# Kernel tuning notes

Hardware: AMD Instinct MI355X
Metric: run time of the kernel (lower is better)

Reference implementation:

```python
import jax, jax.numpy as jnp
import numpy as np

N_NODES = 100000
N_EDGES = 1600000
N_GRAPHS = 256
D_IN = 128
D_HID = 128
D_OUT = 10
N_GIN_LAYERS = 4  # num_layers - 1
BN_EPS = 1e-5


def setup_inputs() -> dict:
    key = jax.random.key(0)
    ks = jax.random.split(key, 16)
    x = jax.random.normal(ks[0], (N_NODES, D_IN), dtype=jnp.float32)
    edge_src = jax.random.randint(ks[1], (N_EDGES,), 0, N_NODES)
    edge_dst = jax.random.randint(ks[2], (N_EDGES,), 0, N_NODES)
    graph_ids = jnp.sort(jax.random.randint(ks[3], (N_NODES,), 0, N_GRAPHS))
    s = 1.0 / np.sqrt(D_HID)
    # stacked per-layer params (all layers 128->128 since input_dim == hidden_dim)
    W1 = jax.random.normal(ks[4], (N_GIN_LAYERS, D_HID, D_HID), dtype=jnp.float32) * s
    b1 = jnp.zeros((N_GIN_LAYERS, D_HID), dtype=jnp.float32)
    g1 = jnp.ones((N_GIN_LAYERS, D_HID), dtype=jnp.float32)
    bt1 = jnp.zeros((N_GIN_LAYERS, D_HID), dtype=jnp.float32)
    W2 = jax.random.normal(ks[5], (N_GIN_LAYERS, D_HID, D_HID), dtype=jnp.float32) * s
    b2 = jnp.zeros((N_GIN_LAYERS, D_HID), dtype=jnp.float32)
    g2 = jnp.ones((N_GIN_LAYERS, D_HID), dtype=jnp.float32)
    bt2 = jnp.zeros((N_GIN_LAYERS, D_HID), dtype=jnp.float32)
    eps = jnp.zeros((N_GIN_LAYERS,), dtype=jnp.float32)          # learn_eps params
    fusion_w = jnp.ones((N_GIN_LAYERS,), dtype=jnp.float32)      # self.weight
    Wp = jax.random.normal(ks[6], (D_HID, D_OUT), dtype=jnp.float32) * s
    bp = jnp.zeros((D_OUT,), dtype=jnp.float32)
    return {"x": x, "edge_src": edge_src, "edge_dst": edge_dst, "graph_ids": graph_ids,
            "eps": eps, "fusion_w": fusion_w, "W1": W1, "b1": b1, "g1": g1, "bt1": bt1,
            "W2": W2, "b2": b2, "g2": g2, "bt2": bt2, "Wp": Wp, "bp": bp}


def _batchnorm(h, gamma, beta):
    # training-mode BatchNorm1d over node axis
    m = jnp.mean(h, axis=0)
    v = jnp.var(h, axis=0)
    return (h - m) * jax.lax.rsqrt(v + BN_EPS) * gamma + beta


def reference(x, edge_src, edge_dst, graph_ids, eps, fusion_w,
              W1, b1, g1, bt1, W2, b2, g2, bt2, Wp, bp):
    h = x
    hiddens = []
    for l in range(N_GIN_LAYERS):
        # sum neighbor aggregation (spmm with learn_eps -> no self loops in Adj)
        pooled = jax.ops.segment_sum(h[edge_src], edge_dst, num_segments=N_NODES)
        pooled = pooled + (1.0 + eps[l]) * h
        # 2-layer MLP: Linear -> BN -> ReLU -> Linear
        t = jax.nn.relu(_batchnorm(pooled @ W1[l] + b1[l], g1[l], bt1[l]))
        t = t @ W2[l] + b2[l]
        # outer BatchNorm + ReLU
        h = jax.nn.relu(_batchnorm(t, g2[l], bt2[l]))
        hiddens.append(h)
    # attention_global, attention_type == 'weight': weighted sum of 4 hidden scales
    fused = (fusion_w[0] * hiddens[0] + fusion_w[1] * hiddens[1]
             + fusion_w[2] * hiddens[2] + fusion_w[3] * hiddens[3])
    # graph sum pooling (graph_pool spmm) then final linear (dropout = eval identity)
    pooled_g = jax.ops.segment_sum(fused, graph_ids, num_segments=N_GRAPHS)
    return pooled_g @ Wp + bp
```

## Files before the change

kernel.cpp:

```cpp
#include <hip/hip_runtime.h>

#define D 128
#define DOUT 10
#define CT_STRIDE 152
#define TSTR 136

typedef float f32x4 __attribute__((ext_vector_type(4)));
typedef __bf16 bf16x8 __attribute__((ext_vector_type(8)));
typedef unsigned short u16;

__device__ __forceinline__ float bf2f(u16 u) {
    return __uint_as_float(((unsigned int)u) << 16);
}
__device__ __forceinline__ u16 f2bf(float f) {
    unsigned int u = __float_as_uint(f);
    u += 0x7fffu + ((u >> 16) & 1u);
    return (u16)(u >> 16);
}

__global__ void k_zero(float4* __restrict__ p, int n4) {
    int i = blockIdx.x * 256 + threadIdx.x;
    if (i < n4) p[i] = make_float4(0.f, 0.f, 0.f, 0.f);
}

__global__ __launch_bounds__(256) void k_prepw(const float* __restrict__ W1,
                                               const float* __restrict__ W2,
                                               bf16x8* __restrict__ wswz, int L) {
    int b = blockIdx.x >> 3;
    const float* W = (b < L) ? (W1 + (size_t)b * D * D)
                             : (W2 + (size_t)(b - L) * D * D);
    bf16x8* o = wswz + (size_t)b * 2048;
    int idx = ((blockIdx.x & 7) << 8) + threadIdx.x;
    int lane_s = idx & 63;
    int f = idx >> 6;
    int n = ((f >> 2) << 4) | (lane_s & 15);
    int kb = ((f & 3) << 5) | ((lane_s >> 4) << 3);
    bf16x8 fr;
#pragma unroll
    for (int j = 0; j < 8; ++j) fr[j] = (__bf16)W[(kb + j) * D + n];
    o[idx] = fr;
}

__global__ __launch_bounds__(256) void k_hist(const int* __restrict__ dst,
                                              int* __restrict__ cnts, int E, int nb) {
    __shared__ int hist[1024];
    int tid = threadIdx.x;
    for (int i = tid; i < nb; i += 256) hist[i] = 0;
    __syncthreads();
    int e0 = blockIdx.x << 11;
    int e1 = e0 + 2048; if (e1 > E) e1 = E;
// ... 16 lines not shown
#pragma unroll
        for (int off = 1; off < 64; off <<= 1) {
            int v = __shfl_up(c, off);
            if (lane >= off) c += v;
        }
        if (idx < nbk) cnts[(idx << 10) + b] = carry + (c - orig);
        carry += __shfl(c, 63);
    }
    if (lane == 0) btot[b] = carry;
}

__global__ __launch_bounds__(256) void k_scat(const int* __restrict__ src,
                                              const int* __restrict__ dst,
                                              const int* __restrict__ cnts,
                                              int* __restrict__ pairs, int E, int nb) {
    __shared__ int lbase[1024];
    __shared__ int lcur[1024];
    int tid = threadIdx.x;
    for (int i = tid; i < nb; i += 256) {
        lbase[i] = cnts[(blockIdx.x << 10) + i];
        lcur[i] = 0;
    }
    __syncthreads();
    int e0 = blockIdx.x << 11;
    int e1 = e0 + 2048; if (e1 > E) e1 = E;
    for (int e = e0 + tid; e < e1; e += 256) {
        int d = dst[e];
        int b = d >> 7;
        int pos = lbase[b] + atomicAdd(&lcur[b], 1);
        if (pos < 4096) pairs[(b << 12) + pos] = (src[e] << 7) | (d & 127);
    }
}

__global__ void k_cvt(const float* __restrict__ x, u16* __restrict__ o,
                      int M, int Mpad) {
    long e = ((long)blockIdx.x * 256 + threadIdx.x) * 4;
    if (e >= (long)Mpad * D) return;
    ushort4 r;
    if (e < (long)M * D) {
        float4 v = *(const float4*)(x + e);
        r.x = f2bf(v.x); r.y = f2bf(v.y); r.z = f2bf(v.z); r.w = f2bf(v.w);
    } else {
        r = make_ushort4(0, 0, 0, 0);
    }
    *(ushort4*)(o + e) = r;
}

__global__ __launch_bounds__(512, 6) void k_aggemm(
        const u16* __restrict__ h, const int* __restrict__ pairs,
        const int* __restrict__ bcnt, const float* __restrict__ eps, int layer,
        const bf16x8* __restrict__ wz, const float* __restrict__ bias,
        u16* __restrict__ O, float* __restrict__ stats, int M, int b0) {
    __shared__ union UA {
        struct { int lcnt[128]; int loff[128]; int lcur[128]; int ledge[4096]; } csr;
        u16 tile[128 * TSTR];
    } shA;
    __shared__ float blds[D], psum[8 * D], psq[8 * D];
    int tid = threadIdx.x;

    if (tid < 128) shA.csr.lcnt[tid] = 0;
    if (tid >= 256 && tid < 256 + D) blds[tid - 256] = bias[tid - 256];
    __syncthreads();

    int b = b0 + blockIdx.x;
    int cnt = bcnt[b];
    if (cnt > 4096) cnt = 4096;
    const int* pb = pairs + ((size_t)b << 12);

    for (int e = tid; e < cnt; e += 512)
        atomicAdd(&shA.csr.lcnt[pb[e] & 127], 1);
    __syncthreads();
    if (tid < 128) shA.csr.loff[tid] = shA.csr.lcnt[tid];
    __syncthreads();
    for (int off = 1; off < 128; off <<= 1) {
        int v = 0;
        if (tid < 128 && tid >= off) v = shA.csr.loff[tid - off];
        __syncthreads();
        if (tid < 128) shA.csr.loff[tid] += v;
        __syncthreads();
    }
    if (tid < 128) shA.csr.lcur[tid] = shA.csr.loff[tid] - shA.csr.lcnt[tid];
    __syncthreads();
    for (int e = tid; e < cnt; e += 512) {
        int p = pb[e];
        int pos = atomicAdd(&shA.csr.lcur[p & 127], 1);
        shA.csr.ledge[pos] = p >> 7;
    }
    __syncthreads();

    float e1 = 1.0f + eps[layer];
    int grp = tid >> 5;
    int c = (tid & 31) << 2;
    float r0[8], r1[8], r2[8], r3[8];
    for (int pass = 0; pass < 8; ++pass) {
        int row = (pass << 4) + grp;
        int node = (b << 7) + row;
        float a0 = 0.f, a1 = 0.f, a2 = 0.f, a3 = 0.f;
        if (node < M) {
            ushort4 sv = *(const ushort4*)(h + ((size_t)node << 7) + c);
            a0 = e1 * bf2f(sv.x); a1 = e1 * bf2f(sv.y);
            a2 = e1 * bf2f(sv.z); a3 = e1 * bf2f(sv.w);
            int dd = shA.csr.lcnt[row];
            int s = shA.csr.loff[row] - dd;
            int i = 0;
            for (; i + 8 <= dd; i += 8) {
                int n0 = shA.csr.ledge[s + i],     n1 = shA.csr.ledge[s + i + 1];
                int n2 = shA.csr.ledge[s + i + 2], n3 = shA.csr.ledge[s + i + 3];
                int n4 = shA.csr.ledge[s + i + 4], n5 = shA.csr.ledge[s + i + 5];
                int n6 = shA.csr.ledge[s + i + 6], n7 = shA.csr.ledge[s + i + 7];
                ushort4 u0 = *(const ushort4*)(h + ((size_t)n0 << 7) + c);
                ushort4 u1 = *(const ushort4*)(h + ((size_t)n1 << 7) + c);
                ushort4 u2 = *(const ushort4*)(h + ((size_t)n2 << 7) + c);
                ushort4 u3 = *(const ushort4*)(h + ((size_t)n3 << 7) + c);
                ushort4 u4 = *(const ushort4*)(h + ((size_t)n4 << 7) + c);
                ushort4 u5 = *(const ushort4*)(h + ((size_t)n5 << 7) + c);
                ushort4 u6 = *(const ushort4*)(h + ((size_t)n6 << 7) + c);
                ushort4 u7 = *(const ushort4*)(h + ((size_t)n7 << 7) + c);
                a0 += bf2f(u0.x) + bf2f(u1.x) + bf2f(u2.x) + bf2f(u3.x)
                    + bf2f(u4.x) + bf2f(u5.x) + bf2f(u6.x) + bf2f(u7.x);
                a1 += bf2f(u0.y) + bf2f(u1.y) + bf2f(u2.y) + bf2f(u3.y)
                    + bf2f(u4.y) + bf2f(u5.y) + bf2f(u6.y) + bf2f(u7.y);
                a2 += bf2f(u0.z) + bf2f(u1.z) + bf2f(u2.z) + bf2f(u3.z)
                    + bf2f(u4.z) + bf2f(u5.z) + bf2f(u6.z) + bf2f(u7.z);
                a3 += bf2f(u0.w) + bf2f(u1.w) + bf2f(u2.w) + bf2f(u3.w)
                    + bf2f(u4.w) + bf2f(u5.w) + bf2f(u6.w) + bf2f(u7.w);
            }
            for (; i + 4 <= dd; i += 4) {
                int n0 = shA.csr.ledge[s + i],     n1 = shA.csr.ledge[s + i + 1];
                int n2 = shA.csr.ledge[s + i + 2], n3 = shA.csr.ledge[s + i + 3];
                ushort4 u0 = *(const ushort4*)(h + ((size_t)n0 << 7) + c);
                ushort4 u1 = *(const ushort4*)(h + ((size_t)n1 << 7) + c);
                ushort4 u2 = *(const ushort4*)(h + ((size_t)n2 << 7) + c);
                ushort4 u3 = *(const ushort4*)(h + ((size_t)n3 << 7) + c);
                a0 += bf2f(u0.x) + bf2f(u1.x) + bf2f(u2.x) + bf2f(u3.x);
                a1 += bf2f(u0.y) + bf2f(u1.y) + bf2f(u2.y) + bf2f(u3.y);
                a2 += bf2f(u0.z) + bf2f(u1.z) + bf2f(u2.z) + bf2f(u3.z);
                a3 += bf2f(u0.w) + bf2f(u1.w) + bf2f(u2.w) + bf2f(u3.w);
            }
            for (; i < dd; ++i) {
                int n0 = shA.csr.ledge[s + i];
                ushort4 u0 = *(const ushort4*)(h + ((size_t)n0 << 7) + c);
                a0 += bf2f(u0.x); a1 += bf2f(u0.y); a2 += bf2f(u0.z); a3 += bf2f(u0.w);
            }
        }
        r0[pass] = a0; r1[pass] = a1; r2[pass] = a2; r3[pass] = a3;
    }
    __syncthreads();

#pragma unroll
    for (int pass = 0; pass < 8; ++pass) {
        int row = (pass << 4) + grp;
        ushort4 v;
        v.x = f2bf(r0[pass]); v.y = f2bf(r1[pass]);
        v.z = f2bf(r2[pass]); v.w = f2bf(r3[pass]);
        *(ushort4*)&shA.tile[row * TSTR + c] = v;
    }
    __syncthreads();

    int wave = tid >> 6, lane = tid & 63;
    int m = lane & 15, quad = lane >> 4;
    f32x4 z = {0.f, 0.f, 0.f, 0.f};
    f32x4 acc[8];
#pragma unroll
    for (int t = 0; t < 8; ++t) acc[t] = z;
    const bf16x8* wl = wz + lane;
#pragma unroll
    for (int kc = 0; kc < 4; ++kc) {
        bf16x8 af = *(const bf16x8*)&shA.tile[(wave * 16 + m) * TSTR + (kc << 5) + (quad << 3)];
        bf16x8 w0 = wl[(0  | kc) << 6];
        bf16x8 w1 = wl[(4  | kc) << 6];
        bf16x8 w2 = wl[(8  | kc) << 6];
        bf16x8 w3 = wl[(12 | kc) << 6];
        acc[0] = __builtin_amdgcn_mfma_f32_16x16x32_bf16(af, w0, acc[0], 0, 0, 0);
        acc[1] = __builtin_amdgcn_mfma_f32_16x16x32_bf16(af, w1, acc[1], 0, 0, 0);
        acc[2] = __builtin_amdgcn_mfma_f32_16x16x32_bf16(af, w2, acc[2], 0, 0, 0);
        acc[3] = __builtin_amdgcn_mfma_f32_16x16x32_bf16(af, w3, acc[3], 0, 0, 0);
        w0 = wl[(16 | kc) << 6];
        w1 = wl[(20 | kc) << 6];
        w2 = wl[(24 | kc) << 6];
        w3 = wl[(28 | kc) << 6];
        acc[4] = __builtin_amdgcn_mfma_f32_16x16x32_bf16(af, w0, acc[4], 0, 0, 0);
        acc[5] = __builtin_amdgcn_mfma_f32_16x16x32_bf16(af, w1, acc[5], 0, 0, 0);
        acc[6] = __builtin_amdgcn_mfma_f32_16x16x32_bf16(af, w2, acc[6], 0, 0, 0);
        acc[7] = __builtin_amdgcn_mfma_f32_16x16x32_bf16(af, w3, acc[7], 0, 0, 0);
    }
    __syncthreads();

    int lr0 = wave * 16 + (quad << 2);
    int gr0 = (b << 7) + lr0;
#pragma unroll
    for (int t = 0; t < 8; ++t) {
        int cch = (t << 4) | m;
        float bc = blds[cch];
        float s = 0.f, q = 0.f;
#pragma unroll
        for (int r = 0; r < 4; ++r) {
            float v = acc[t][r] + bc;
            shA.tile[(lr0 + r) * TSTR + cch] = f2bf(v);
            if (gr0 + r < M) { s += v; q += v * v; }
        }
        s += __shfl_xor(s, 16); s += __shfl_xor(s, 32);
        q += __shfl_xor(q, 16); q += __shfl_xor(q, 32);
        if (quad == 0) { psum[wave * D + cch] = s; psq[wave * D + cch] = q; }
    }
    __syncthreads();

    int mrow = M - (b << 7);
#pragma unroll
    for (int i = 0; i < 4; ++i) {
        int idx = (i << 9) + tid;
        int row = idx >> 4, ch8 = (idx & 15) << 3;
        if (row < mrow) {
            float4 v = *(const float4*)&shA.tile[row * TSTR + ch8];
            *(float4*)(O + (((size_t)(b << 7) + row) << 7) + ch8) = v;
        }
    }
    if (tid < D) {
        float s = 0.f, q = 0.f;
#pragma unroll
        for (int w = 0; w < 8; ++w) { s += psum[w * D + tid]; q += psq[w * D + tid]; }
        float* st = stats + ((b & 7) << 8);
        atomicAdd(&st[tid], s);
        atomicAdd(&st[D + tid], q);
    }
}

__global__ __launch_bounds__(256, 4) void k_gemm_bn(
        u16* __restrict__ A, const bf16x8* __restrict__ wz,
        const float* __restrict__ bias, const float* __restrict__ stats_in,
        const float* __restrict__ gamma, const float* __restrict__ beta,
        float* __restrict__ stats_out, float invM, int M) {
    __shared__ union { bf16x8 w[2048]; u16 c[64 * CT_STRIDE]; } sh;
    __shared__ float blds[D], s_sc[D], s_sh[D], psum[4 * D], psq[4 * D];
    int tid = threadIdx.x;
    int wave = tid >> 6, lane = tid & 63;
    int m = lane & 15, quad = lane >> 4;
    int row0 = blockIdx.x * 64 + wave * 16;

    const u16* ap = A + (size_t)(row0 + m) * D + (quad << 3);
    ushort4 p[4][2];
#pragma unroll
    for (int kc = 0; kc < 4; ++kc) {
        p[kc][0] = *(const ushort4*)(ap + (kc << 5));
        p[kc][1] = *(const ushort4*)(ap + (kc << 5) + 4);
    }

    for (int i = tid; i < 2048; i += 256) sh.w[i] = wz[i];
    if (tid < D) {
        float s = 0.f, q = 0.f;
#pragma unroll
        for (int r = 0; r < 8; ++r) {
            s += stats_in[(r << 8) + tid];
            q += stats_in[(r << 8) + D + tid];
        }
        float mean = s * invM;
        float var = q * invM - mean * mean;
        float sc = rsqrtf(var + 1e-5f) * gamma[tid];
        s_sc[tid] = sc;
        s_sh[tid] = beta[tid] - mean * sc;
        blds[tid] = bias[tid];
    }
    __syncthreads();

    f32x4 z = {0.f, 0.f, 0.f, 0.f};
    f32x4 acc[8];
#pragma unroll
    for (int t = 0; t < 8; ++t) acc[t] = z;

#pragma unroll
    for (int kc = 0; kc < 4; ++kc) {
        int kb = (kc << 5) | (quad << 3);
        float4 c0 = *(const float4*)&s_sc[kb];
// ... 13 lines not shown
#pragma unroll
        for (int t = 0; t < 8; ++t)
            acc[t] = __builtin_amdgcn_mfma_f32_16x16x32_bf16(
                af, sh.w[(((t << 2) | kc) << 6) | lane], acc[t], 0, 0, 0);
    }
    __syncthreads();

    int lr0 = wave * 16 + (quad << 2);
    int gr0 = blockIdx.x * 64 + lr0;
#pragma unroll
    for (int t = 0; t < 8; ++t) {
        int cch = (t << 4) | m;
        float bc = blds[cch];
        float s = 0.f, q = 0.f;
#pragma unroll
        for (int r = 0; r < 4; ++r) {
            float v = acc[t][r] + bc;
            sh.c[(lr0 + r) * CT_STRIDE + cch] = f2bf(v);
            if (gr0 + r < M) { s += v; q += v * v; }
        }
        s += __shfl_xor(s, 16); s += __shfl_xor(s, 32);
        q += __shfl_xor(q, 16); q += __shfl_xor(q, 32);
        if (quad == 0) { psum[wave * D + cch] = s; psq[wave * D + cch] = q; }
    }
    __syncthreads();

    int mrow = M - blockIdx.x * 64;
#pragma unroll
    for (int i = 0; i < 4; ++i) {
        int idx = (i << 8) + tid;
        int row = idx >> 4, ch8 = (idx & 15) << 3;
        if (row < mrow) {
            float4 v = *(const float4*)&sh.c[row * CT_STRIDE + ch8];
            *(float4*)(A + ((size_t)(blockIdx.x * 64 + row) << 7) + ch8) = v;
        }
    }
    if (tid < D) {
        float s = psum[tid] + psum[D + tid] + psum[2 * D + tid] + psum[3 * D + tid];
        float q = psq[tid] + psq[D + tid] + psq[2 * D + tid] + psq[3 * D + tid];
        float* st = stats_out + ((blockIdx.x & 7) << 8);
        atomicAdd(&st[tid], s);
        atomicAdd(&st[D + tid], q);
    }
}

__global__ __launch_bounds__(256) void k_bn2pool(
        const u16* __restrict__ y, const float* __restrict__ stats,
        const float* __restrict__ gamma, const float* __restrict__ beta,
        const int* __restrict__ gids, const float* __restrict__ fw,
        int layer, u16* __restrict__ hout, float* __restrict__ gacc,
        float invM, int M) {
    __shared__ float s_sc[D], s_sh[D];
    int t = threadIdx.x;
    if (t < D) {
        float s = 0.f, q = 0.f;
#pragma unroll
        for (int r = 0; r < 8; ++r) {
            s += stats[(r << 8) + t];
            q += stats[(r << 8) + D + t];
        }
        float mean = s * invM;
        float sv = rsqrtf(q * invM - mean * mean + 1e-5f) * gamma[t];
        s_sc[t] = sv;
        s_sh[t] = beta[t] - mean * sv;
    }
    __syncthreads();

    int c = (t & 31) << 2;
    int strip = t >> 5;
    long base = (long)blockIdx.x * 64 + (long)strip * 8;
    if (base >= M) return;
    float4 sc4 = *(const float4*)&s_sc[c];
    float4 sh4 = *(const float4*)&s_sh[c];

    ushort4 v[8];
#pragma unroll
    for (int r = 0; r < 8; ++r)
        v[r] = *(const ushort4*)(y + ((base + r) << 7) + c);
    long gmax = (long)M - 1;
    int g[8];
#pragma unroll
    for (int r = 0; r < 8; ++r) {
        long idx = base + r;
        g[r] = gids[idx > gmax ? gmax : idx];
    }

    float h0[8], h1[8], h2[8], h3[8];
#pragma unroll
    for (int r = 0; r < 8; ++r) {
        h0[r] = fmaxf(0.f, fmaf(bf2f(v[r].x), sc4.x, sh4.x));
        h1[r] = fmaxf(0.f, fmaf(bf2f(v[r].y), sc4.y, sh4.y));
        h2[r] = fmaxf(0.f, fmaf(bf2f(v[r].z), sc4.z, sh4.z));
        h3[r] = fmaxf(0.f, fmaf(bf2f(v[r].w), sc4.w, sh4.w));
    }
#pragma unroll
    for (int r = 0; r < 8; ++r) {
        if (base + r < M) {
            ushort4 o;
            o.x = f2bf(h0[r]); o.y = f2bf(h1[r]);
            o.z = f2bf(h2[r]); o.w = f2bf(h3[r]);
            *(ushort4*)(hout + ((base + r) << 7) + c) = o;
        }
    }

    float wl = fw[layer];
    int cur = -1;
    float a0 = 0.f, a1 = 0.f, a2 = 0.f, a3 = 0.f;
#pragma unroll
    for (int r = 0; r < 8; ++r) {
        if (base + r < M) {
            if (g[r] != cur) {
                if (cur >= 0) {
                    float* gp = gacc + ((size_t)cur << 7) + c;
                    atomicAdd(gp, wl * a0); atomicAdd(gp + 1, wl * a1);
                    atomicAdd(gp + 2, wl * a2); atomicAdd(gp + 3, wl * a3);
                }
                cur = g[r];
                a0 = a1 = a2 = a3 = 0.f;
            }
            a0 += h0[r]; a1 += h1[r]; a2 += h2[r]; a3 += h3[r];
        }
    }
    if (cur >= 0) {
        float* gp = gacc + ((size_t)cur << 7) + c;
        atomicAdd(gp, wl * a0); atomicAdd(gp + 1, wl * a1);
        atomicAdd(gp + 2, wl * a2); atomicAdd(gp + 3, wl * a3);
    }
}

__global__ void k_final(const float* __restrict__ gacc, const float* __restrict__ Wp,
                        const float* __restrict__ bp, float* __restrict__ out) {
    __shared__ float w[D * DOUT];
    __shared__ float bb[DOUT];
    int t = threadIdx.x;
    for (int i = t; i < D * DOUT; i += blockDim.x) w[i] = Wp[i];
    if (t < DOUT) bb[t] = bp[t];
    __syncthreads();
    float acc[DOUT];
#pragma unroll
    for (int o = 0; o < DOUT; ++o) acc[o] = bb[o];
    for (int k = 0; k < D; ++k) {
        float a = gacc[(size_t)t * D + k];
#pragma unroll
        for (int o = 0; o < DOUT; ++o) acc[o] += a * w[k * DOUT + o];
    }
#pragma unroll
    for (int o = 0; o < DOUT; ++o) out[(size_t)t * DOUT + o] = acc[o];
}

extern "C" void kernel_launch(void* const* d_in, const int* in_sizes, int n_in,
                              void* d_out, int out_size, void* d_ws, size_t ws_size,
                              hipStream_t stream) {
    const float* x    = (const float*)d_in[0];
    const int* esrc   = (const int*)d_in[1];
    const int* edst   = (const int*)d_in[2];
    const int* gids   = (const int*)d_in[3];
    const float* eps  = (const float*)d_in[4];
    const float* fw   = (const float*)d_in[5];
    const float* W1   = (const float*)d_in[6];
    const float* b1   = (const float*)d_in[7];
    const float* g1   = (const float*)d_in[8];
    const float* bt1  = (const float*)d_in[9];
    const float* W2   = (const float*)d_in[10];
    const float* b2   = (const float*)d_in[11];
    const float* g2   = (const float*)d_in[12];
    const float* bt2  = (const float*)d_in[13];
    const float* Wp   = (const float*)d_in[14];
    const float* bp   = (const float*)d_in[15];
    float* out        = (float*)d_out;

    const int M = in_sizes[3];
    const int E = in_sizes[1];
    const int L = in_sizes[4];
    const int G = out_size / DOUT;
    const int nb  = (M + 127) >> 7;
    const int Mpad = nb << 7;
    const int nbk = (E + 2047) >> 11;
    const float invM = 1.0f / (float)M;

    char* ws = (char*)d_ws;
    u16* bufT  = (u16*)ws;  ws += (size_t)Mpad * D * 2;
    u16* bufH  = (u16*)ws;  ws += (size_t)Mpad * D * 2;
    int* pairs = (int*)ws;  ws += (size_t)nb * 4096 * 4;
    int* cnts  = (int*)ws;  ws += (size_t)nbk * 1024 * 4;
    int* btot  = (int*)ws;  ws += 1024 * 4;
    bf16x8* wswz = (bf16x8*)ws; ws += (size_t)2 * L * 2048 * 16;
    float* stats = (float*)ws; ws += (size_t)L * 4096 * 4;
    float* gacc  = (float*)ws; ws += (size_t)G * D * 4;

    int zbytes = L * 4096 * 4 + G * D * 4;
    int n4 = zbytes / 16;
    k_zero<<<(n4 + 255) / 256, 256, 0, stream>>>((float4*)stats, n4);

    k_prepw<<<2 * L * 8, 256, 0, stream>>>(W1, W2, wswz, L);
    k_hist<<<nbk, 256, 0, stream>>>(edst, cnts, E, nb);
    k_off<<<(nb + 3) / 4, 256, 0, stream>>>(cnts, btot, nbk, nb);
    k_scat<<<nbk, 256, 0, stream>>>(esrc, edst, cnts, pairs, E, nb);
    k_cvt<<<(Mpad * (D / 4) + 255) / 256, 256, 0, stream>>>(x, bufH, M, Mpad);

    int pool_grid = (M + 63) / 64;
    for (int l = 0; l < L; ++l) {
        float* st1 = stats + (size_t)l * 4096;
        float* st2 = st1 + 2048;
        k_aggemm<<<nb, 512, 0, stream>>>(bufH, pairs, btot, eps, l,
                                         wswz + (size_t)l * 2048, b1 + (size_t)l * D,
                                         bufT, st1, M, 0);
        k_gemm_bn<<<Mpad / 64, 256, 0, stream>>>(bufT, wswz + (size_t)(L + l) * 2048,
                                                 b2 + (size_t)l * D, st1,
                                                 g1 + (size_t)l * D, bt1 + (size_t)l * D,
                                                 st2, invM, M);
        k_bn2pool<<<pool_grid, 256, 0, stream>>>(bufT, st2, g2 + (size_t)l * D,
                                                 bt2 + (size_t)l * D, gids, fw, l,
                                                 bufH, gacc, invM, M);
    }
    k_final<<<1, G, 0, stream>>>(gacc, Wp, bp, out);
}
```

Measured before the change: 758.0 us.

## Fuse outer BatchNorm+ReLU and graph pooling into next layer's aggregation kernel

The separate BN2+ReLU+pool kernel is removed for all but the last layer. Its work moves into the next layer's aggregation gather, which now applies the previous layer's scale/shift and ReLU to each gathered neighbor row on the fly and accumulates graph pooling from self rows. k_gemm_bn writes its pre-BN output straight into the H buffer, and the aggregation kernel becomes persistent with a capped grid looping over buckets. This saves one full read/write pass over the node features per layer and one launch per layer. In exchange it adds FMA+ReLU per gathered element (about 16x redundant across edges) and extra shared memory.

```diff
diff --git a/kernel.cpp b/kernel.cpp
--- a/kernel.cpp
+++ b/kernel.cpp
@@ -16,6 +16,18 @@
     unsigned int u = __float_as_uint(f);
     u += 0x7fffu + ((u >> 16) & 1u);
     return (u16)(u >> 16);
+}
+
+__device__ __forceinline__ float4 cvt4(ushort4 u, float4 sc, float4 sh, bool fly) {
+    float4 r;
+    r.x = bf2f(u.x); r.y = bf2f(u.y); r.z = bf2f(u.z); r.w = bf2f(u.w);
+    if (fly) {
+        r.x = fmaxf(0.f, fmaf(r.x, sc.x, sh.x));
+        r.y = fmaxf(0.f, fmaf(r.y, sc.y, sh.y));
+        r.z = fmaxf(0.f, fmaf(r.z, sc.z, sh.z));
+        r.w = fmaxf(0.f, fmaf(r.w, sc.w, sh.w));
+    }
+    return r;
 }
 
 __global__ void k_zero(float4* __restrict__ p, int n4) {
@@ -112,187 +124,249 @@
     *(ushort4*)(o + e) = r;
 }
 
+template<int FLY>
 __global__ __launch_bounds__(512, 6) void k_aggemm(
         const u16* __restrict__ h, const int* __restrict__ pairs,
         const int* __restrict__ bcnt, const float* __restrict__ eps, int layer,
         const bf16x8* __restrict__ wz, const float* __restrict__ bias,
-        u16* __restrict__ O, float* __restrict__ stats, int M, int b0) {
+        u16* __restrict__ O, float* __restrict__ stats, int M, int nbuck,
+        const float* __restrict__ st2, const float* __restrict__ g2,
+        const float* __restrict__ bt2, const int* __restrict__ gids,
+        const float* __restrict__ fw, float* __restrict__ gacc, float invM) {
     __shared__ union UA {
         struct { int lcnt[128]; int loff[128]; int lcur[128]; int ledge[4096]; } csr;
         u16 tile[128 * TSTR];
     } shA;
     __shared__ float blds[D], psum[8 * D], psq[8 * D];
+    __shared__ float s_sc2[D], s_sh2[D];
+    __shared__ int gidl[128];
     int tid = threadIdx.x;
 
-    if (tid < 128) shA.csr.lcnt[tid] = 0;
-    if (tid >= 256 && tid < 256 + D) blds[tid - 256] = bias[tid - 256];
-    __syncthreads();
-
-    int b = b0 + blockIdx.x;
-    int cnt = bcnt[b];
-    if (cnt > 4096) cnt = 4096;
-    const int* pb = pairs + ((size_t)b << 12);
-
-    for (int e = tid; e < cnt; e += 512)
-        atomicAdd(&shA.csr.lcnt[pb[e] & 127], 1);
-    __syncthreads();
-    if (tid < 128) shA.csr.loff[tid] = shA.csr.lcnt[tid];
-    __syncthreads();
-    for (int off = 1; off < 128; off <<= 1) {
-        int v = 0;
-        if (tid < 128 && tid >= off) v = shA.csr.loff[tid - off];
-        __syncthreads();
-        if (tid < 128) shA.csr.loff[tid] += v;
-        __syncthreads();
-    }
-    if (tid < 128) shA.csr.lcur[tid] = shA.csr.loff[tid] - shA.csr.lcnt[tid];
-    __syncthreads();
-    for (int e = tid; e < cnt; e += 512) {
-        int p = pb[e];
-        int pos = atomicAdd(&shA.csr.lcur[p & 127], 1);
-        shA.csr.ledge[pos] = p >> 7;
-    }
-    __syncthreads();
-
-    float e1 = 1.0f + eps[layer];
+    if (tid < D) {
+        blds[tid] = bias[tid];
+        if (FLY) {
+            float s = 0.f, q = 0.f;
+#pragma unroll
+            for (int r = 0; r < 8; ++r) {
+                s += st2[(r << 8) + tid];
+                q += st2[(r << 8) + D + tid];
+            }
+            float mean = s * invM;
+            float sc = rsqrtf(q * invM - mean * mean + 1e-5f) * g2[tid];
+            s_sc2[tid] = sc;
+            s_sh2[tid] = bt2[tid] - mean * sc;
+        }
+    }
+    __syncthreads();
+
     int grp = tid >> 5;
     int c = (tid & 31) << 2;
-    float r0[8], r1[8], r2[8], r3[8];
-    for (int pass = 0; pass < 8; ++pass) {
-        int row = (pass << 4) + grp;
-        int node = (b << 7) + row;
-        float a0 = 0.f, a1 = 0.f, a2 = 0.f, a3 = 0.f;
-        if (node < M) {
-            ushort4 sv = *(const ushort4*)(h + ((size_t)node << 7) + c);
-            a0 = e1 * bf2f(sv.x); a1 = e1 * bf2f(sv.y);
-            a2 = e1 * bf2f(sv.z); a3 = e1 * bf2f(sv.w);
-            int dd = shA.csr.lcnt[row];
-            int s = shA.csr.loff[row] - dd;
-            int i = 0;
-            for (; i + 8 <= dd; i += 8) {
-                int n0 = shA.csr.ledge[s + i],     n1 = shA.csr.ledge[s + i + 1];
-                int n2 = shA.csr.ledge[s + i + 2], n3 = shA.csr.ledge[s + i + 3];
-                int n4 = shA.csr.ledge[s + i + 4], n5 = shA.csr.ledge[s + i + 5];
-                int n6 = shA.csr.ledge[s + i + 6], n7 = shA.csr.ledge[s + i + 7];
-                ushort4 u0 = *(const ushort4*)(h + ((size_t)n0 << 7) + c);
-                ushort4 u1 = *(const ushort4*)(h + ((size_t)n1 << 7) + c);
-                ushort4 u2 = *(const ushort4*)(h + ((size_t)n2 << 7) + c);
-                ushort4 u3 = *(const ushort4*)(h + ((size_t)n3 << 7) + c);
-                ushort4 u4 = *(const ushort4*)(h + ((size_t)n4 << 7) + c);
-                ushort4 u5 = *(const ushort4*)(h + ((size_t)n5 << 7) + c);
-                ushort4 u6 = *(const ushort4*)(h + ((size_t)n6 << 7) + c);
-                ushort4 u7 = *(const ushort4*)(h + ((size_t)n7 << 7) + c);
-                a0 += bf2f(u0.x) + bf2f(u1.x) + bf2f(u2.x) + bf2f(u3.x)
-                    + bf2f(u4.x) + bf2f(u5.x) + bf2f(u6.x) + bf2f(u7.x);
-                a1 += bf2f(u0.y) + bf2f(u1.y) + bf2f(u2.y) + bf2f(u3.y)
-                    + bf2f(u4.y) + bf2f(u5.y) + bf2f(u6.y) + bf2f(u7.y);
-                a2 += bf2f(u0.z) + bf2f(u1.z) + bf2f(u2.z) + bf2f(u3.z)
-                    + bf2f(u4.z) + bf2f(u5.z) + bf2f(u6.z) + bf2f(u7.z);
-                a3 += bf2f(u0.w) + bf2f(u1.w) + bf2f(u2.w) + bf2f(u3.w)
-                    + bf2f(u4.w) + bf2f(u5.w) + bf2f(u6.w) + bf2f(u7.w);
-            }
-            for (; i + 4 <= dd; i += 4) {
-                int n0 = shA.csr.ledge[s + i],     n1 = shA.csr.ledge[s + i + 1];
-                int n2 = shA.csr.ledge[s + i + 2], n3 = shA.csr.ledge[s + i + 3];
-                ushort4 u0 = *(const ushort4*)(h + ((size_t)n0 << 7) + c);
-                ushort4 u1 = *(const ushort4*)(h + ((size_t)n1 << 7) + c);
-                ushort4 u2 = *(const ushort4*)(h + ((size_t)n2 << 7) + c);
-                ushort4 u3 = *(const ushort4*)(h + ((size_t)n3 << 7) + c);
-                a0 += bf2f(u0.x) + bf2f(u1.x) + bf2f(u2.x) + bf2f(u3.x);
-                a1 += bf2f(u0.y) + bf2f(u1.y) + bf2f(u2.y) + bf2f(u3.y);
-                a2 += bf2f(u0.z) + bf2f(u1.z) + bf2f(u2.z) + bf2f(u3.z);
-                a3 += bf2f(u0.w) + bf2f(u1.w) + bf2f(u2.w) + bf2f(u3.w);
-            }
-            for (; i < dd; ++i) {
-                int n0 = shA.csr.ledge[s + i];
-                ushort4 u0 = *(const ushort4*)(h + ((size_t)n0 << 7) + c);
-                a0 += bf2f(u0.x); a1 += bf2f(u0.y); a2 += bf2f(u0.z); a3 += bf2f(u0.w);
-            }
-        }
-        r0[pass] = a0; r1[pass] = a1; r2[pass] = a2; r3[pass] = a3;
-    }
-    __syncthreads();
-
-#pragma unroll
-    for (int pass = 0; pass < 8; ++pass) {
-        int row = (pass << 4) + grp;
-        ushort4 v;
-        v.x = f2bf(r0[pass]); v.y = f2bf(r1[pass]);
-        v.z = f2bf(r2[pass]); v.w = f2bf(r3[pass]);
-        *(ushort4*)&shA.tile[row * TSTR + c] = v;
-    }
-    __syncthreads();
-
+    float4 scv = make_float4(1.f, 1.f, 1.f, 1.f);
+    float4 shv = make_float4(0.f, 0.f, 0.f, 0.f);
+    float wl = 0.f;
+    if (FLY) {
+        scv = *(const float4*)&s_sc2[c];
+        shv = *(const float4*)&s_sh2[c];
+        wl = fw[layer - 1];
+    }
+    float e1 = 1.0f + eps[layer];
     int wave = tid >> 6, lane = tid & 63;
     int m = lane & 15, quad = lane >> 4;
-    f32x4 z = {0.f, 0.f, 0.f, 0.f};
-    f32x4 acc[8];
-#pragma unroll
-    for (int t = 0; t < 8; ++t) acc[t] = z;
-    const bf16x8* wl = wz + lane;
-#pragma unroll
-    for (int kc = 0; kc < 4; ++kc) {
-        bf16x8 af = *(const bf16x8*)&shA.tile[(wave * 16 + m) * TSTR + (kc << 5) + (quad << 3)];
-        bf16x8 w0 = wl[(0  | kc) << 6];
-        bf16x8 w1 = wl[(4  | kc) << 6];
-        bf16x8 w2 = wl[(8  | kc) << 6];
-        bf16x8 w3 = wl[(12 | kc) << 6];
-        acc[0] = __builtin_amdgcn_mfma_f32_16x16x32_bf16(af, w0, acc[0], 0, 0, 0);
-        acc[1] = __builtin_amdgcn_mfma_f32_16x16x32_bf16(af, w1, acc[1], 0, 0, 0);
-        acc[2] = __builtin_amdgcn_mfma_f32_16x16x32_bf16(af, w2, acc[2], 0, 0, 0);
-        acc[3] = __builtin_amdgcn_mfma_f32_16x16x32_bf16(af, w3, acc[3], 0, 0, 0);
-        w0 = wl[(16 | kc) << 6];
-        w1 = wl[(20 | kc) << 6];
-        w2 = wl[(24 | kc) << 6];
-        w3 = wl[(28 | kc) << 6];
-        acc[4] = __builtin_amdgcn_mfma_f32_16x16x32_bf16(af, w0, acc[4], 0, 0, 0);
-        acc[5] = __builtin_amdgcn_mfma_f32_16x16x32_bf16(af, w1, acc[5], 0, 0, 0);
-        acc[6] = __builtin_amdgcn_mfma_f32_16x16x32_bf16(af, w2, acc[6], 0, 0, 0);
-        acc[7] = __builtin_amdgcn_mfma_f32_16x16x32_bf16(af, w3, acc[7], 0, 0, 0);
-    }
-    __syncthreads();
-
-    int lr0 = wave * 16 + (quad << 2);
-    int gr0 = (b << 7) + lr0;
-#pragma unroll
-    for (int t = 0; t < 8; ++t) {
-        int cch = (t << 4) | m;
-        float bc = blds[cch];
-        float s = 0.f, q = 0.f;
-#pragma unroll
-        for (int r = 0; r < 4; ++r) {
-            float v = acc[t][r] + bc;
-            shA.tile[(lr0 + r) * TSTR + cch] = f2bf(v);
-            if (gr0 + r < M) { s += v; q += v * v; }
-        }
-        s += __shfl_xor(s, 16); s += __shfl_xor(s, 32);
-        q += __shfl_xor(q, 16); q += __shfl_xor(q, 32);
-        if (quad == 0) { psum[wave * D + cch] = s; psq[wave * D + cch] = q; }
-    }
-    __syncthreads();
-
-    int mrow = M - (b << 7);
-#pragma unroll
-    for (int i = 0; i < 4; ++i) {
-        int idx = (i << 9) + tid;
-        int row = idx >> 4, ch8 = (idx & 15) << 3;
-        if (row < mrow) {
-            float4 v = *(const float4*)&shA.tile[row * TSTR + ch8];
-            *(float4*)(O + (((size_t)(b << 7) + row) << 7) + ch8) = v;
-        }
-    }
-    if (tid < D) {
-        float s = 0.f, q = 0.f;
-#pragma unroll
-        for (int w = 0; w < 8; ++w) { s += psum[w * D + tid]; q += psq[w * D + tid]; }
-        float* st = stats + ((b & 7) << 8);
-        atomicAdd(&st[tid], s);
-        atomicAdd(&st[D + tid], q);
+
+    for (int b = blockIdx.x; b < nbuck; b += gridDim.x) {
+        __syncthreads();
+
+        if (tid < 128) shA.csr.lcnt[tid] = 0;
+        if (FLY && tid >= 128 && tid < 256) {
+            int node = (b << 7) + (tid - 128);
+            gidl[tid - 128] = (node < M) ? gids[node] : -1;
+        }
+        __syncthreads();
+
+        int cnt = bcnt[b];
+        if (cnt > 4096) cnt = 4096;
+        const int* pb = pairs + ((size_t)b << 12);
+
+        for (int e = tid; e < cnt; e += 512)
+            atomicAdd(&shA.csr.lcnt[pb[e] & 127], 1);
+        __syncthreads();
+        if (tid < 128) shA.csr.loff[tid] = shA.csr.lcnt[tid];
+        __syncthreads();
+        for (int off = 1; off < 128; off <<= 1) {
+            int v = 0;
+            if (tid < 128 && tid >= off) v = shA.csr.loff[tid - off];
+            __syncthreads();
+            if (tid < 128) shA.csr.loff[tid] += v;
+            __syncthreads();
+        }
+        if (tid < 128) shA.csr.lcur[tid] = shA.csr.loff[tid] - shA.csr.lcnt[tid];
+        __syncthreads();
+        for (int e = tid; e < cnt; e += 512) {
+            int p = pb[e];
+            int pos = atomicAdd(&shA.csr.lcur[p & 127], 1);
+            shA.csr.ledge[pos] = p >> 7;
+        }
+        __syncthreads();
+
+        float r0[8], r1[8], r2[8], r3[8];
+        int curg = -1;
+        float p0 = 0.f, p1 = 0.f, p2 = 0.f, p3 = 0.f;
+        for (int pass = 0; pass < 8; ++pass) {
+            int row = (pass << 4) + grp;
+            int node = (b << 7) + row;
+            float a0 = 0.f, a1 = 0.f, a2 = 0.f, a3 = 0.f;
+            if (node < M) {
+                ushort4 sv = *(const ushort4*)(h + ((size_t)node << 7) + c);
+                float4 hs = cvt4(sv, scv, shv, FLY);
+                if (FLY) {
+                    int g = gidl[row];
+                    if (g != curg) {
+                        if (curg >= 0) {
+                            float* gp = gacc + ((size_t)curg << 7) + c;
+                            atomicAdd(gp, wl * p0); atomicAdd(gp + 1, wl * p1);
+                            atomicAdd(gp + 2, wl * p2); atomicAdd(gp + 3, wl * p3);
+                        }
+                        curg = g;
+                        p0 = p1 = p2 = p3 = 0.f;
+                    }
+                    p0 += hs.x; p1 += hs.y; p2 += hs.z; p3 += hs.w;
+                }
+                a0 = e1 * hs.x; a1 = e1 * hs.y; a2 = e1 * hs.z; a3 = e1 * hs.w;
+                int dd = shA.csr.lcnt[row];
+                int s = shA.csr.loff[row] - dd;
+                int i = 0;
+                for (; i + 8 <= dd; i += 8) {
+                    int n0 = shA.csr.ledge[s + i],     n1 = shA.csr.ledge[s + i + 1];
+                    int n2 = shA.csr.ledge[s + i + 2], n3 = shA.csr.ledge[s + i + 3];
+                    int n4 = shA.csr.ledge[s + i + 4], n5 = shA.csr.ledge[s + i + 5];
+                    int n6 = shA.csr.ledge[s + i + 6], n7 = shA.csr.ledge[s + i + 7];
+                    ushort4 u0 = *(const ushort4*)(h + ((size_t)n0 << 7) + c);
+                    ushort4 u1 = *(const ushort4*)(h + ((size_t)n1 << 7) + c);
+                    ushort4 u2 = *(const ushort4*)(h + ((size_t)n2 << 7) + c);
+                    ushort4 u3 = *(const ushort4*)(h + ((size_t)n3 << 7) + c);
+                    ushort4 u4 = *(const ushort4*)(h + ((size_t)n4 << 7) + c);
+                    ushort4 u5 = *(const ushort4*)(h + ((size_t)n5 << 7) + c);
+                    ushort4 u6 = *(const ushort4*)(h + ((size_t)n6 << 7) + c);
+                    ushort4 u7 = *(const ushort4*)(h + ((size_t)n7 << 7) + c);
+                    float4 v0 = cvt4(u0, scv, shv, FLY), v1 = cvt4(u1, scv, shv, FLY);
+                    float4 v2 = cvt4(u2, scv, shv, FLY), v3 = cvt4(u3, scv, shv, FLY);
+                    float4 v4 = cvt4(u4, scv, shv, FLY), v5 = cvt4(u5, scv, shv, FLY);
+                    float4 v6 = cvt4(u6, scv, shv, FLY), v7 = cvt4(u7, scv, shv, FLY);
+                    a0 += v0.x + v1.x + v2.x + v3.x + v4.x + v5.x + v6.x + v7.x;
+                    a1 += v0.y + v1.y + v2.y + v3.y + v4.y + v5.y + v6.y + v7.y;
+                    a2 += v0.z + v1.z + v2.z + v3.z + v4.z + v5.z + v6.z + v7.z;
+                    a3 += v0.w + v1.w + v2.w + v3.w + v4.w + v5.w + v6.w + v7.w;
+                }
+                for (; i + 4 <= dd; i += 4) {
+                    int n0 = shA.csr.ledge[s + i],     n1 = shA.csr.ledge[s + i + 1];
+                    int n2 = shA.csr.ledge[s + i + 2], n3 = shA.csr.ledge[s + i + 3];
+                    ushort4 u0 = *(const ushort4*)(h + ((size_t)n0 << 7) + c);
+                    ushort4 u1 = *(const ushort4*)(h + ((size_t)n1 << 7) + c);
+                    ushort4 u2 = *(const ushort4*)(h + ((size_t)n2 << 7) + c);
+                    ushort4 u3 = *(const ushort4*)(h + ((size_t)n3 << 7) + c);
+                    float4 v0 = cvt4(u0, scv, shv, FLY), v1 = cvt4(u1, scv, shv, FLY);
+                    float4 v2 = cvt4(u2, scv, shv, FLY), v3 = cvt4(u3, scv, shv, FLY);
+                    a0 += v0.x + v1.x + v2.x + v3.x;
+                    a1 += v0.y + v1.y + v2.y + v3.y;
+                    a2 += v0.z + v1.z + v2.z + v3.z;
+                    a3 += v0.w + v1.w + v2.w + v3.w;
+                }
+                for (; i < dd; ++i) {
+                    int n0 = shA.csr.ledge[s + i];
+                    ushort4 u0 = *(const ushort4*)(h + ((size_t)n0 << 7) + c);
+                    float4 v0 = cvt4(u0, scv, shv, FLY);
+                    a0 += v0.x; a1 += v0.y; a2 += v0.z; a3 += v0.w;
+                }
+            }
+            r0[pass] = a0; r1[pass] = a1; r2[pass] = a2; r3[pass] = a3;
+        }
+        if (FLY && curg >= 0) {
+            float* gp = gacc + ((size_t)curg << 7) + c;
+            atomicAdd(gp, wl * p0); atomicAdd(gp + 1, wl * p1);
+            atomicAdd(gp + 2, wl * p2); atomicAdd(gp + 3, wl * p3);
+        }
+        __syncthreads();
+
+#pragma unroll
+        for (int pass = 0; pass < 8; ++pass) {
+            int row = (pass << 4) + grp;
+            ushort4 v;
+            v.x = f2bf(r0[pass]); v.y = f2bf(r1[pass]);
+            v.z = f2bf(r2[pass]); v.w = f2bf(r3[pass]);
+            *(ushort4*)&shA.tile[row * TSTR + c] = v;
+        }
+        __syncthreads();
+
+        f32x4 z = {0.f, 0.f, 0.f, 0.f};
+        f32x4 acc[8];
+#pragma unroll
+        for (int t = 0; t < 8; ++t) acc[t] = z;
+        const bf16x8* wlp = wz + lane;
+#pragma unroll
+        for (int kc = 0; kc < 4; ++kc) {
+            bf16x8 af = *(const bf16x8*)&shA.tile[(wave * 16 + m) * TSTR + (kc << 5) + (quad << 3)];
+            bf16x8 w0 = wlp[(0  | kc) << 6];
+            bf16x8 w1 = wlp[(4  | kc) << 6];
+            bf16x8 w2 = wlp[(8  | kc) << 6];
+            bf16x8 w3 = wlp[(12 | kc) << 6];
+            acc[0] = __builtin_amdgcn_mfma_f32_16x16x32_bf16(af, w0, acc[0], 0, 0, 0);
+            acc[1] = __builtin_amdgcn_mfma_f32_16x16x32_bf16(af, w1, acc[1], 0, 0, 0);
+            acc[2] = __builtin_amdgcn_mfma_f32_16x16x32_bf16(af, w2, acc[2], 0, 0, 0);
+            acc[3] = __builtin_amdgcn_mfma_f32_16x16x32_bf16(af, w3, acc[3], 0, 0, 0);
+            w0 = wlp[(16 | kc) << 6];
+            w1 = wlp[(20 | kc) << 6];
+            w2 = wlp[(24 | kc) << 6];
+            w3 = wlp[(28 | kc) << 6];
+            acc[4] = __builtin_amdgcn_mfma_f32_16x16x32_bf16(af, w0, acc[4], 0, 0, 0);
+            acc[5] = __builtin_amdgcn_mfma_f32_16x16x32_bf16(af, w1, acc[5], 0, 0, 0);
+            acc[6] = __builtin_amdgcn_mfma_f32_16x16x32_bf16(af, w2, acc[6], 0, 0, 0);
+            acc[7] = __builtin_amdgcn_mfma_f32_16x16x32_bf16(af, w3, acc[7], 0, 0, 0);
+        }
+        __syncthreads();
+
+        int lr0 = wave * 16 + (quad << 2);
+        int gr0 = (b << 7) + lr0;
+#pragma unroll
+        for (int t = 0; t < 8; ++t) {
+            int cch = (t << 4) | m;
+            float bc = blds[cch];
+            float s = 0.f, q = 0.f;
+#pragma unroll
+            for (int r = 0; r < 4; ++r) {
+                float v = acc[t][r] + bc;
+                shA.tile[(lr0 + r) * TSTR + cch] = f2bf(v);
+                if (gr0 + r < M) { s += v; q += v * v; }
+            }
+            s += __shfl_xor(s, 16); s += __shfl_xor(s, 32);
+            q += __shfl_xor(q, 16); q += __shfl_xor(q, 32);
+            if (quad == 0) { psum[wave * D + cch] = s; psq[wave * D + cch] = q; }
+        }
+        __syncthreads();
+
+        int mrow = M - (b << 7);
+#pragma unroll
+        for (int i = 0; i < 4; ++i) {
+            int idx = (i << 9) + tid;
+            int row = idx >> 4, ch8 = (idx & 15) << 3;
+            if (row < mrow) {
+                float4 v = *(const float4*)&shA.tile[row * TSTR + ch8];
+                *(float4*)(O + (((size_t)(b << 7) + row) << 7) + ch8) = v;
+            }
+        }
+        if (tid < D) {
+            float s = 0.f, q = 0.f;
+#pragma unroll
+            for (int w = 0; w < 8; ++w) { s += psum[w * D + tid]; q += psq[w * D + tid]; }
+            float* st = stats + ((b & 7) << 8);
+            atomicAdd(&st[tid], s);
+            atomicAdd(&st[D + tid], q);
+        }
     }
 }
 
 __global__ __launch_bounds__(256, 4) void k_gemm_bn(
-        u16* __restrict__ A, const bf16x8* __restrict__ wz,
+        const u16* __restrict__ Ain, u16* __restrict__ Aout,
+        const bf16x8* __restrict__ wz,
         const float* __restrict__ bias, const float* __restrict__ stats_in,
         const float* __restrict__ gamma, const float* __restrict__ beta,
         float* __restrict__ stats_out, float invM, int M) {
@@ -303,7 +377,7 @@
     int m = lane & 15, quad = lane >> 4;
     int row0 = blockIdx.x * 64 + wave * 16;
 
-    const u16* ap = A + (size_t)(row0 + m) * D + (quad << 3);
+    const u16* ap = Ain + (size_t)(row0 + m) * D + (quad << 3);
     ushort4 p[4][2];
 #pragma unroll
     for (int kc = 0; kc < 4; ++kc) {
@@ -383,7 +457,7 @@
         int row = idx >> 4, ch8 = (idx & 15) << 3;
         if (row < mrow) {
             float4 v = *(const float4*)&sh.c[row * CT_STRIDE + ch8];
-            *(float4*)(A + ((size_t)(blockIdx.x * 64 + row) << 7) + ch8) = v;
+            *(float4*)(Aout + ((size_t)(blockIdx.x * 64 + row) << 7) + ch8) = v;
         }
     }
     if (tid < D) {
@@ -395,12 +469,11 @@
     }
 }
 
-__global__ __launch_bounds__(256) void k_bn2pool(
+__global__ __launch_bounds__(256) void k_pool(
         const u16* __restrict__ y, const float* __restrict__ stats,
         const float* __restrict__ gamma, const float* __restrict__ beta,
         const int* __restrict__ gids, const float* __restrict__ fw,
-        int layer, u16* __restrict__ hout, float* __restrict__ gacc,
-        float invM, int M) {
+        int layer, float* __restrict__ gacc, float invM, int M) {
     __shared__ float s_sc[D], s_sh[D];
     int t = threadIdx.x;
     if (t < D) {
@@ -443,15 +516,6 @@
         h1[r] = fmaxf(0.f, fmaf(bf2f(v[r].y), sc4.y, sh4.y));
         h2[r] = fmaxf(0.f, fmaf(bf2f(v[r].z), sc4.z, sh4.z));
         h3[r] = fmaxf(0.f, fmaf(bf2f(v[r].w), sc4.w, sh4.w));
-    }
-#pragma unroll
-    for (int r = 0; r < 8; ++r) {
-        if (base + r < M) {
-            ushort4 o;
-            o.x = f2bf(h0[r]); o.y = f2bf(h1[r]);
-            o.z = f2bf(h2[r]); o.w = f2bf(h3[r]);
-            *(ushort4*)(hout + ((base + r) << 7) + c) = o;
-        }
     }
 
     float wl = fw[layer];
@@ -549,20 +613,34 @@
     k_scat<<<nbk, 256, 0, stream>>>(esrc, edst, cnts, pairs, E, nb);
     k_cvt<<<(Mpad * (D / 4) + 255) / 256, 256, 0, stream>>>(x, bufH, M, Mpad);
 
-    int pool_grid = (M + 63) / 64;
+    int ag = nb < 768 ? nb : 768;
     for (int l = 0; l < L; ++l) {
         float* st1 = stats + (size_t)l * 4096;
         float* st2 = st1 + 2048;
-        k_aggemm<<<nb, 512, 0, stream>>>(bufH, pairs, btot, eps, l,
-                                         wswz + (size_t)l * 2048, b1 + (size_t)l * D,
-                                         bufT, st1, M, 0);
-        k_gemm_bn<<<Mpad / 64, 256, 0, stream>>>(bufT, wswz + (size_t)(L + l) * 2048,
+        if (l == 0) {
+            k_aggemm<0><<<ag, 512, 0, stream>>>(bufH, pairs, btot, eps, l,
+                                                wswz + (size_t)l * 2048, b1 + (size_t)l * D,
+                                                bufT, st1, M, nb,
+                                                stats, g2, bt2, gids, fw, gacc, invM);
+        } else {
+            float* st2p = stats + (size_t)(l - 1) * 4096 + 2048;
+            k_aggemm<1><<<ag, 512, 0, stream>>>(bufH, pairs, btot, eps, l,
+                                                wswz + (size_t)l * 2048, b1 + (size_t)l * D,
+                                                bufT, st1, M, nb,
+                                                st2p, g2 + (size_t)(l - 1) * D,
+                                                bt2 + (size_t)(l - 1) * D, gids, fw,
+                                                gacc, invM);
+        }
+        k_gemm_bn<<<Mpad / 64, 256, 0, stream>>>(bufT, bufH,
+                                                 wswz + (size_t)(L + l) * 2048,
                                                  b2 + (size_t)l * D, st1,
                                                  g1 + (size_t)l * D, bt1 + (size_t)l * D,
                                                  st2, invM, M);
-        k_bn2pool<<<pool_grid, 256, 0, stream>>>(bufT, st2, g2 + (size_t)l * D,
-                                                 bt2 + (size_t)l * D, gids, fw, l,
-                                                 bufH, gacc, invM, M);
-    }
+    }
+    float* st2last = stats + (size_t)(L - 1) * 4096 + 2048;
+    k_pool<<<(M + 63) / 64, 256, 0, stream>>>(bufH, st2last,
+                                              g2 + (size_t)(L - 1) * D,
+                                              bt2 + (size_t)(L - 1) * D,
+                                              gids, fw, L - 1, gacc, invM, M);
     k_final<<<1, G, 0, stream>>>(gacc, Wp, bp, out);
 }
```

Measured after the change: 1.351 ms. 78.2% more time.

## Restructure BN+pool kernel to one block per graph segment without atomics

Applied to the files above, without the earlier changes.

Graph segment boundaries are precomputed by binary search over the sorted graph ids. The BN2+ReLU+pool kernel then runs one 512-thread block per graph, which reduces rows in shared memory and adds to gacc without atomics. The last layer skips writing the hidden activations because no later layer reads them. The catch is that the grid shrinks to only G=256 blocks of uneven size, which could hurt bandwidth utilisation and load balance.

```diff
diff --git a/kernel.cpp b/kernel.cpp
--- a/kernel.cpp
+++ b/kernel.cpp
@@ -98,6 +98,19 @@
     }
 }
 
+__global__ void k_gseg(const int* __restrict__ gids, int* __restrict__ gptr,
+                       int M, int G) {
+    int g = blockIdx.x * blockDim.x + threadIdx.x;
+    if (g > G) return;
+    if (g == 0) { gptr[0] = 0; return; }
+    int lo = 0, hi = M;
+    while (lo < hi) {
+        int mid = (lo + hi) >> 1;
+        if (gids[mid] < g) lo = mid + 1; else hi = mid;
+    }
+    gptr[g] = lo;
+}
+
 __global__ void k_cvt(const float* __restrict__ x, u16* __restrict__ o,
                       int M, int Mpad) {
     long e = ((long)blockIdx.x * 256 + threadIdx.x) * 4;
@@ -116,7 +129,7 @@
         const u16* __restrict__ h, const int* __restrict__ pairs,
         const int* __restrict__ bcnt, const float* __restrict__ eps, int layer,
         const bf16x8* __restrict__ wz, const float* __restrict__ bias,
-        u16* __restrict__ O, float* __restrict__ stats, int M, int b0) {
+        u16* __restrict__ O, float* __restrict__ stats, int M) {
     __shared__ union UA {
         struct { int lcnt[128]; int loff[128]; int lcur[128]; int ledge[4096]; } csr;
         u16 tile[128 * TSTR];
@@ -128,7 +141,7 @@
     if (tid >= 256 && tid < 256 + D) blds[tid - 256] = bias[tid - 256];
     __syncthreads();
 
-    int b = b0 + blockIdx.x;
+    int b = blockIdx.x;
     int cnt = bcnt[b];
     if (cnt > 4096) cnt = 4096;
     const int* pb = pairs + ((size_t)b << 12);
@@ -229,22 +242,22 @@
     f32x4 acc[8];
 #pragma unroll
     for (int t = 0; t < 8; ++t) acc[t] = z;
-    const bf16x8* wl = wz + lane;
+    const bf16x8* wlp = wz + lane;
 #pragma unroll
     for (int kc = 0; kc < 4; ++kc) {
         bf16x8 af = *(const bf16x8*)&shA.tile[(wave * 16 + m) * TSTR + (kc << 5) + (quad << 3)];
-        bf16x8 w0 = wl[(0  | kc) << 6];
-        bf16x8 w1 = wl[(4  | kc) << 6];
-        bf16x8 w2 = wl[(8  | kc) << 6];
-        bf16x8 w3 = wl[(12 | kc) << 6];
+        bf16x8 w0 = wlp[(0  | kc) << 6];
+        bf16x8 w1 = wlp[(4  | kc) << 6];
+        bf16x8 w2 = wlp[(8  | kc) << 6];
+        bf16x8 w3 = wlp[(12 | kc) << 6];
         acc[0] = __builtin_amdgcn_mfma_f32_16x16x32_bf16(af, w0, acc[0], 0, 0, 0);
         acc[1] = __builtin_amdgcn_mfma_f32_16x16x32_bf16(af, w1, acc[1], 0, 0, 0);
         acc[2] = __builtin_amdgcn_mfma_f32_16x16x32_bf16(af, w2, acc[2], 0, 0, 0);
         acc[3] = __builtin_amdgcn_mfma_f32_16x16x32_bf16(af, w3, acc[3], 0, 0, 0);
-        w0 = wl[(16 | kc) << 6];
-        w1 = wl[(20 | kc) << 6];
-        w2 = wl[(24 | kc) << 6];
-        w3 = wl[(28 | kc) << 6];
+        w0 = wlp[(16 | kc) << 6];
+        w1 = wlp[(20 | kc) << 6];
+        w2 = wlp[(24 | kc) << 6];
+        w3 = wlp[(28 | kc) << 6];
         acc[4] = __builtin_amdgcn_mfma_f32_16x16x32_bf16(af, w0, acc[4], 0, 0, 0);
         acc[5] = __builtin_amdgcn_mfma_f32_16x16x32_bf16(af, w1, acc[5], 0, 0, 0);
         acc[6] = __builtin_amdgcn_mfma_f32_16x16x32_bf16(af, w2, acc[6], 0, 0, 0);
@@ -395,13 +408,31 @@
     }
 }
 
-__global__ __launch_bounds__(256) void k_bn2pool(
+__device__ __forceinline__ void bnrow(const u16* __restrict__ y,
+                                      u16* __restrict__ hout, size_t row, int c,
+                                      float4 sc4, float4 sh4, int writeh,
+                                      float& a0, float& a1, float& a2, float& a3) {
+    ushort4 u = *(const ushort4*)(y + (row << 7) + c);
+    float h0 = fmaxf(0.f, fmaf(bf2f(u.x), sc4.x, sh4.x));
+    float h1 = fmaxf(0.f, fmaf(bf2f(u.y), sc4.y, sh4.y));
+    float h2 = fmaxf(0.f, fmaf(bf2f(u.z), sc4.z, sh4.z));
+    float h3 = fmaxf(0.f, fmaf(bf2f(u.w), sc4.w, sh4.w));
+    if (writeh) {
+        ushort4 o;
+        o.x = f2bf(h0); o.y = f2bf(h1); o.z = f2bf(h2); o.w = f2bf(h3);
+        *(ushort4*)(hout + (row << 7) + c) = o;
+    }
+    a0 += h0; a1 += h1; a2 += h2; a3 += h3;
+}
+
+template<int WRITEH>
+__global__ __launch_bounds__(512) void k_bnpool(
         const u16* __restrict__ y, const float* __restrict__ stats,
         const float* __restrict__ gamma, const float* __restrict__ beta,
-        const int* __restrict__ gids, const float* __restrict__ fw,
-        int layer, u16* __restrict__ hout, float* __restrict__ gacc,
-        float invM, int M) {
+        const int* __restrict__ gptr, const float* __restrict__ fw,
+        int layer, u16* __restrict__ hout, float* __restrict__ gacc, float invM) {
     __shared__ float s_sc[D], s_sh[D];
+    __shared__ float red[16 * D];
     int t = threadIdx.x;
     if (t < D) {
         float s = 0.f, q = 0.f;
@@ -417,65 +448,32 @@
     }
     __syncthreads();
 
+    int g = blockIdx.x;
+    int n0 = gptr[g], n1 = gptr[g + 1];
     int c = (t & 31) << 2;
-    int strip = t >> 5;
-    long base = (long)blockIdx.x * 64 + (long)strip * 8;
-    if (base >= M) return;
+    int rg = t >> 5;
     float4 sc4 = *(const float4*)&s_sc[c];
     float4 sh4 = *(const float4*)&s_sh[c];
 
-    ushort4 v[8];
-#pragma unroll
-    for (int r = 0; r < 8; ++r)
-        v[r] = *(const ushort4*)(y + ((base + r) << 7) + c);
-    long gmax = (long)M - 1;
-    int g[8];
-#pragma unroll
-    for (int r = 0; r < 8; ++r) {
-        long idx = base + r;
-        g[r] = gids[idx > gmax ? gmax : idx];
-    }
-
-    float h0[8], h1[8], h2[8], h3[8];
-#pragma unroll
-    for (int r = 0; r < 8; ++r) {
-        h0[r] = fmaxf(0.f, fmaf(bf2f(v[r].x), sc4.x, sh4.x));
-        h1[r] = fmaxf(0.f, fmaf(bf2f(v[r].y), sc4.y, sh4.y));
-        h2[r] = fmaxf(0.f, fmaf(bf2f(v[r].z), sc4.z, sh4.z));
-        h3[r] = fmaxf(0.f, fmaf(bf2f(v[r].w), sc4.w, sh4.w));
-    }
-#pragma unroll
-    for (int r = 0; r < 8; ++r) {
-        if (base + r < M) {
-            ushort4 o;
-            o.x = f2bf(h0[r]); o.y = f2bf(h1[r]);
-            o.z = f2bf(h2[r]); o.w = f2bf(h3[r]);
-            *(ushort4*)(hout + ((base + r) << 7) + c) = o;
-        }
-    }
-
-    float wl = fw[layer];
-    int cur = -1;
     float a0 = 0.f, a1 = 0.f, a2 = 0.f, a3 = 0.f;
-#pragma unroll
-    for (int r = 0; r < 8; ++r) {
-        if (base + r < M) {
-            if (g[r] != cur) {
-                if (cur >= 0) {
-                    float* gp = gacc + ((size_t)cur << 7) + c;
-                    atomicAdd(gp, wl * a0); atomicAdd(gp + 1, wl * a1);
-                    atomicAdd(gp + 2, wl * a2); atomicAdd(gp + 3, wl * a3);
-                }
-                cur = g[r];
-                a0 = a1 = a2 = a3 = 0.f;
-            }
-            a0 += h0[r]; a1 += h1[r]; a2 += h2[r]; a3 += h3[r];
-        }
-    }
-    if (cur >= 0) {
-        float* gp = gacc + ((size_t)cur << 7) + c;
-        atomicAdd(gp, wl * a0); atomicAdd(gp + 1, wl * a1);
-        atomicAdd(gp + 2, wl * a2); atomicAdd(gp + 3, wl * a3);
+    int r = n0 + rg;
+    for (; r + 48 < n1; r += 64) {
+        bnrow(y, hout, (size_t)r,        c, sc4, sh4, WRITEH, a0, a1, a2, a3);
+        bnrow(y, hout, (size_t)(r + 16), c, sc4, sh4, WRITEH, a0, a1, a2, a3);
+        bnrow(y, hout, (size_t)(r + 32), c, sc4, sh4, WRITEH, a0, a1, a2, a3);
+        bnrow(y, hout, (size_t)(r + 48), c, sc4, sh4, WRITEH, a0, a1, a2, a3);
+    }
+    for (; r < n1; r += 16)
+        bnrow(y, hout, (size_t)r, c, sc4, sh4, WRITEH, a0, a1, a2, a3);
+
+    *(float4*)&red[rg * D + c] = make_float4(a0, a1, a2, a3);
+    __syncthreads();
+
+    if (t < D) {
+        float s = 0.f;
+#pragma unroll
+        for (int w = 0; w < 16; ++w) s += red[w * D + t];
+        gacc[((size_t)g << 7) + t] += fw[layer] * s;
     }
 }
 
@@ -535,6 +533,7 @@
     int* pairs = (int*)ws;  ws += (size_t)nb * 4096 * 4;
     int* cnts  = (int*)ws;  ws += (size_t)nbk * 1024 * 4;
     int* btot  = (int*)ws;  ws += 1024 * 4;
+    int* gptr  = (int*)ws;  ws += 512 * 4;
     bf16x8* wswz = (bf16x8*)ws; ws += (size_t)2 * L * 2048 * 16;
     float* stats = (float*)ws; ws += (size_t)L * 4096 * 4;
     float* gacc  = (float*)ws; ws += (size_t)G * D * 4;
@@ -547,22 +546,27 @@
     k_hist<<<nbk, 256, 0, stream>>>(edst, cnts, E, nb);
     k_off<<<(nb + 3) / 4, 256, 0, stream>>>(cnts, btot, nbk, nb);
     k_scat<<<nbk, 256, 0, stream>>>(esrc, edst, cnts, pairs, E, nb);
+    k_gseg<<<1, 512, 0, stream>>>(gids, gptr, M, G);
     k_cvt<<<(Mpad * (D / 4) + 255) / 256, 256, 0, stream>>>(x, bufH, M, Mpad);
 
-    int pool_grid = (M + 63) / 64;
     for (int l = 0; l < L; ++l) {
         float* st1 = stats + (size_t)l * 4096;
         float* st2 = st1 + 2048;
         k_aggemm<<<nb, 512, 0, stream>>>(bufH, pairs, btot, eps, l,
                                          wswz + (size_t)l * 2048, b1 + (size_t)l * D,
-                                         bufT, st1, M, 0);
+                                         bufT, st1, M);
         k_gemm_bn<<<Mpad / 64, 256, 0, stream>>>(bufT, wswz + (size_t)(L + l) * 2048,
                                                  b2 + (size_t)l * D, st1,
                                                  g1 + (size_t)l * D, bt1 + (size_t)l * D,
                                                  st2, invM, M);
-        k_bn2pool<<<pool_grid, 256, 0, stream>>>(bufT, st2, g2 + (size_t)l * D,
-                                                 bt2 + (size_t)l * D, gids, fw, l,
-                                                 bufH, gacc, invM, M);
+        if (l < L - 1)
+            k_bnpool<1><<<G, 512, 0, stream>>>(bufT, st2, g2 + (size_t)l * D,
+                                               bt2 + (size_t)l * D, gptr, fw, l,
+                                               bufH, gacc, invM);
+        else
+            k_bnpool<0><<<G, 512, 0, stream>>>(bufT, st2, g2 + (size_t)l * D,
+                                               bt2 + (size_t)l * D, gptr, fw, l,
+                                               bufH, gacc, invM);
     }
     k_final<<<1, G, 0, stream>>>(gacc, Wp, bp, out);
 }
```

Result: faster. 657.3 us (-13.3%).
